# Optimization experiments

Measured on AMD Instinct MI355X. Metric: run time of the kernel, lower is better.

## Reference

```python
import jax, jax.numpy as jnp
import numpy as np

SAME_RANGE = 0.2  # depth tolerance for averaging splats at the same target pixel


def setup_inputs() -> dict:
    key = jax.random.key(0)
    k1, k2, k3 = jax.random.split(key, 3)
    B, C, H, W = 8, 3, 512, 1024
    obj = jax.random.normal(k1, (B, C, H, W), dtype=jnp.float32)
    flow = jax.random.normal(k2, (B, 2, H, W), dtype=jnp.float32)
    depth = jax.random.uniform(k3, (B, 1, H, W), dtype=jnp.float32)
    return {"obj": obj, "flow": flow, "depth": depth}


def reference(obj, flow, depth):
    # Forward-warping splat with per-target-pixel depth (z-buffer) test.
    # For each source pixel: warp by flow, round to nearest target pixel,
    # keep/average contributions whose depth is within same_range of the
    # minimum depth landing on that target pixel.
    B, C, H, W = obj.shape
    # p0: meshgrid with indexing='xy' stacked as (x, y) channels
    gx = jnp.arange(W, dtype=jnp.float32)[None, :]  # [1, W]
    gy = jnp.arange(H, dtype=jnp.float32)[:, None]  # [H, 1]
    p1x = gx + flow[:, 0]  # [B, H, W]
    p1y = gy + flow[:, 1]
    safe_x = jnp.clip(p1x, 0.0, W - 1)
    safe_y = jnp.clip(p1y, 0.0, H - 1)
    xi = jnp.round(safe_x).astype(jnp.int32)
    yi = jnp.round(safe_y).astype(jnp.int32)
    # flat target index, batch-offset so one segment op covers all batches
    boff = (jnp.arange(B, dtype=jnp.int32) * (H * W))[:, None, None]
    idx = (boff + yi * W + xi).reshape(-1)          # [B*H*W]
    d = depth.reshape(-1)                           # [B*H*W] (depth has 1 channel)
    n_seg = B * H * W
    # z-buffer: per-target minimum depth among all splatted source pixels
    dlut = jax.ops.segment_min(d, idx, num_segments=n_seg)
    # contributions within same_range of the winner are averaged
    keep = (d <= dlut[idx] + SAME_RANGE).astype(obj.dtype)  # [B*H*W]
    vals = obj.transpose(0, 2, 3, 1).reshape(-1, C)         # [B*H*W, C]
    sums = jax.ops.segment_sum(vals * keep[:, None], idx, num_segments=n_seg)
    cnts = jax.ops.segment_sum(keep, idx, num_segments=n_seg)
    out = jnp.where(cnts[:, None] > 0, sums / jnp.maximum(cnts[:, None], 1.0), 0.0)
    return out.reshape(B, H, W, C).transpose(0, 3, 1, 2)
```

## Files before the change

### kernel.cpp

```cpp
#include <hip/hip_runtime.h>

#define BB 8
#define CC 3
#define HH 512
#define WW 1024
#define HW (HH * WW)
#define SAME_RANGE 0.2f

#define R 4
#define TX 64
#define TY 32
#define TT (TX * TY)
#define RX (TX + 2 * R)
#define RY (TY + 2 * R)
#define QX (RX / 4)
#define NSLOT (RY * QX)
#define NTHREADS 768
#define CAP 16384
#define D_SENTINEL 0x7F7F7F7F

#define FP_BIAS  16.0f
#define FP_SCALE 524288.0f
#define FP2_BIAS 8.0f
#define FP2_SCALE 8192.0f

__device__ __forceinline__ unsigned int fp_enc(float v) {
    return (unsigned int)__float2uint_rn((v + FP_BIAS) * FP_SCALE);
}
__device__ __forceinline__ unsigned int fp2_enc(float v) {
    return (unsigned int)__float2uint_rn((v + FP2_BIAS) * FP2_SCALE);
}

__device__ __forceinline__ float f4_get(const float4& v, int j) {
    return j == 0 ? v.x : (j == 1 ? v.y : (j == 2 ? v.z : v.w));
}

__global__ __launch_bounds__(NTHREADS) void gather_kernel(
        const float* __restrict__ obj,
        const float* __restrict__ flow,
        const float* __restrict__ depth,
        int* __restrict__ counter,
        float* __restrict__ list,
        float* __restrict__ out) {
    __shared__ int s_dmin[TT];
    __shared__ unsigned int s_a0[TT];
    __shared__ unsigned int s_a1[TT];
    __shared__ unsigned int s_a2c[TT];

    int lin = blockIdx.x + 16 * blockIdx.y + 256 * blockIdx.z;
    int wgid = (lin & 7) * 256 + (lin >> 3);
    int b   = wgid >> 8;
    int rr  = wgid & 255;
    int tx0 = (rr & 15) * TX;
    int ty0 = (rr >> 4) * TY;
    int tid = threadIdx.x;

    for (int i = tid; i < TT; i += NTHREADS) {
        s_dmin[i] = D_SENTINEL;
        s_a0[i] = 0u;
        s_a1[i] = 0u;
        s_a2c[i] = 0u;
    }
    __syncthreads();

    int    c_rem = -1;
    int    c_tl[4] = {-1, -1, -1, -1};
    float  c_d[4] = {0.f, 0.f, 0.f, 0.f};
    float4 c_o0 = make_float4(0.f, 0.f, 0.f, 0.f);
    float4 c_o1 = make_float4(0.f, 0.f, 0.f, 0.f);
    float4 c_o2 = make_float4(0.f, 0.f, 0.f, 0.f);

    if (tid < NSLOT) {
        int sy = tid / QX;
        int sx4 = tid - sy * QX;
        int gy = ty0 - R + sy;
        int gxb = tx0 - R + (sx4 << 2);
        if (gy >= 0 && gy < HH && gxb >= 0 && gxb < WW) {
            int rem = gy * WW + gxb;
            const float4 fx4 = *reinterpret_cast<const float4*>(flow + (size_t)(b * 2 + 0) * HW + rem);
            const float4 fy4 = *reinterpret_cast<const float4*>(flow + (size_t)(b * 2 + 1) * HW + rem);
            const float4 dd4 = *reinterpret_cast<const float4*>(depth + (size_t)b * HW + rem);
            c_o0 = *reinterpret_cast<const float4*>(obj + (size_t)(b * CC + 0) * HW + rem);
            c_o1 = *reinterpret_cast<const float4*>(obj + (size_t)(b * CC + 1) * HW + rem);
            c_o2 = *reinterpret_cast<const float4*>(obj + (size_t)(b * CC + 2) * HW + rem);
            float gyf = (float)gy;
            c_rem = rem;
            #pragma unroll
            for (int j = 0; j < 4; ++j) {
                int px = gxb + j;
                float fx = f4_get(fx4, j) + (float)px;
                float fy = f4_get(fy4, j) + gyf;
                fx = fminf(fmaxf(fx, 0.0f), (float)(WW - 1));
                fy = fminf(fmaxf(fy, 0.0f), (float)(HH - 1));
                int xi = (int)rintf(fx);
                int yi = (int)rintf(fy);
                int ddx = xi - px; if (ddx < 0) ddx = -ddx;
                int ddy = yi - gy; if (ddy < 0) ddy = -ddy;
                float dj = f4_get(dd4, j);
                if (ddx <= R && ddy <= R) {
                    int lx = xi - tx0;
                    int ly = yi - ty0;
                    if (lx >= 0 && lx < TX && ly >= 0 && ly < TY) {
                        int tloc = ly * TX + lx;
                        c_tl[j] = tloc;
                        c_d[j] = dj;
                        atomicMin(&s_dmin[tloc], __float_as_int(dj));
                    }
                } else if (px >= tx0 && px < tx0 + TX &&
                           gy >= ty0 && gy < ty0 + TY) {
                    int pos = atomicAdd(counter, 1);
                    if (pos < CAP) {
                        float* e = list + (size_t)pos * 8;
                        e[0] = __int_as_float(b * HW + yi * WW + xi);
                        e[1] = dj;
                        e[2] = f4_get(c_o0, j);
                        e[3] = f4_get(c_o1, j);
                        e[4] = f4_get(c_o2, j);
                    }
                }
            }
        }
    }
    __syncthreads();

    if (c_rem >= 0) {
        #pragma unroll
        for (int j = 0; j < 4; ++j) {
            int t = c_tl[j];
            if (t >= 0) {
                float thresh = __int_as_float(s_dmin[t]) + SAME_RANGE;
                if (c_d[j] <= thresh) {
                    atomicAdd(&s_a0[t], fp_enc(f4_get(c_o0, j)));
                    atomicAdd(&s_a1[t], fp_enc(f4_get(c_o1, j)));
                    atomicAdd(&s_a2c[t], fp2_enc(f4_get(c_o2, j)) | (1u << 24));
                }
            }
        }
    }
    __syncthreads();

    if (tid < (TT >> 2)) {
        int base = tid << 2;
        int lx = base & (TX - 1);
        int ly = base >> 6;
        int orow = (ty0 + ly) * WW + tx0 + lx;
        float4 r0, r1, r2;
        #pragma unroll
        for (int k = 0; k < 4; ++k) {
            unsigned int a0 = s_a0[base + k];
            unsigned int a1 = s_a1[base + k];
            unsigned int a2c = s_a2c[base + k];
            unsigned int cnt = a2c >> 24;
            float f0 = 0.0f, f1 = 0.0f, f2 = 0.0f;
            if (cnt > 0) {
                float invc = 1.0f / (float)cnt;
                float inv19 = (1.0f / FP_SCALE) * invc;
                f0 = (float)a0 * inv19 - FP_BIAS;
                f1 = (float)a1 * inv19 - FP_BIAS;
                f2 = (float)(a2c & 0x00ffffffu) * ((1.0f / FP2_SCALE) * invc) - FP2_BIAS;
            }
            ((float*)&r0)[k] = f0;
            ((float*)&r1)[k] = f1;
            ((float*)&r2)[k] = f2;
        }
        *reinterpret_cast<float4*>(out + (size_t)(b * CC + 0) * HW + orow) = r0;
        *reinterpret_cast<float4*>(out + (size_t)(b * CC + 1) * HW + orow) = r1;
        *reinterpret_cast<float4*>(out + (size_t)(b * CC + 2) * HW + orow) = r2;
    }
}

__global__ __launch_bounds__(64) void fixup_kernel(
        const float* __restrict__ obj,
        const float* __restrict__ flow,
        const float* __restrict__ depth,
        const int* __restrict__ counter,
        const float* __restrict__ list,
        float* __restrict__ out) {
    int noutl = *counter;
    if (noutl > CAP) noutl = CAP;
    int lane = threadIdx.x;
    for (int o = blockIdx.x; o < noutl; o += gridDim.x) {
        int tidx = __float_as_int(list[(size_t)o * 8]);
        int tb   = tidx >> 19;
        int trem = tidx & (HW - 1);
        int tyy  = trem >> 10;
        int txx  = trem & (WW - 1);
        float cd[2] = {0.0f, 0.0f};
        int   cr[2] = {-1, -1};
        float dmin = 1e30f;
        #pragma unroll
        for (int c = 0; c < 2; ++c) {
            int k = lane + c * 64;
            if (k < 81) {
                int ky = k / 9;
                int sy = tyy - R + ky;
                int sx = txx - R + (k - ky * 9);
                if (sx >= 0 && sx < WW && sy >= 0 && sy < HH) {
                    int srem = sy * WW + sx;
                    float fx = flow[(tb * 2 + 0) * HW + srem] + (float)sx;
                    float fy = flow[(tb * 2 + 1) * HW + srem] + (float)sy;
                    fx = fminf(fmaxf(fx, 0.0f), (float)(WW - 1));
                    fy = fminf(fmaxf(fy, 0.0f), (float)(HH - 1));
                    if ((int)rintf(fx) == txx && (int)rintf(fy) == tyy) {
                        float d = depth[tb * HW + srem];
                        cd[c] = d; cr[c] = srem;
                        dmin = fminf(dmin, d);
                    }
                }
            }
        }
        for (int k = lane; k < noutl; k += 64) {
            const float* e = list + (size_t)k * 8;
            if (__float_as_int(e[0]) == tidx) dmin = fminf(dmin, e[1]);
        }
        #pragma unroll
        for (int m = 32; m >= 1; m >>= 1)
            dmin = fminf(dmin, __shfl_xor(dmin, m));
        float thr = dmin + SAME_RANGE;
        float s0 = 0.0f, s1 = 0.0f, s2 = 0.0f, cnt = 0.0f;
        #pragma unroll
        for (int c = 0; c < 2; ++c) {
            if (cr[c] >= 0 && cd[c] <= thr) {
                s0 += obj[(tb * CC + 0) * HW + cr[c]];
                s1 += obj[(tb * CC + 1) * HW + cr[c]];
                s2 += obj[(tb * CC + 2) * HW + cr[c]];
                cnt += 1.0f;
            }
        }
        for (int k = lane; k < noutl; k += 64) {
            const float* e = list + (size_t)k * 8;
            if (__float_as_int(e[0]) == tidx && e[1] <= thr) {
                s0 += e[2]; s1 += e[3]; s2 += e[4]; cnt += 1.0f;
            }
        }
        #pragma unroll
        for (int m = 32; m >= 1; m >>= 1) {
            s0  += __shfl_xor(s0, m);
            s1  += __shfl_xor(s1, m);
            s2  += __shfl_xor(s2, m);
            cnt += __shfl_xor(cnt, m);
        }
        if (lane == 0) {
            out[(tb * CC + 0) * HW + trem] = s0 / cnt;
            out[(tb * CC + 1) * HW + trem] = s1 / cnt;
            out[(tb * CC + 2) * HW + trem] = s2 / cnt;
        }
    }
}

extern "C" void kernel_launch(void* const* d_in, const int* in_sizes, int n_in,
                              void* d_out, int out_size, void* d_ws, size_t ws_size,
                              hipStream_t stream) {
    const float* obj   = (const float*)d_in[0];
    const float* flow  = (const float*)d_in[1];
    const float* depth = (const float*)d_in[2];
    float* out = (float*)d_out;

    int*   counter = (int*)d_ws;
    float* list    = (float*)((char*)d_ws + 256);

    hipMemsetAsync(counter, 0, sizeof(int), stream);

    gather_kernel<<<dim3(WW / TX, HH / TY, BB), dim3(NTHREADS), 0, stream>>>(
        obj, flow, depth, counter, list, out);

    fixup_kernel<<<dim3(64), dim3(64), 0, stream>>>(
        obj, flow, depth, counter, list, out);
}
```

Measured before the change: 149.0 us.

## Process two horizontal tiles per workgroup with software-pipelined loads

Each workgroup now handles two adjacent 64x32 tiles using separate shared-memory buffers. The second tile's global loads are issued before the first tile's accumulate and store phases, so memory latency overlaps with shared-memory atomic work. The grid is halved and shared memory per block doubles, which may lower occupancy. Halo pixels shared between the two tiles are still loaded twice.

```diff
diff --git a/kernel.cpp b/kernel.cpp
--- a/kernel.cpp
+++ b/kernel.cpp
@@ -11,6 +11,7 @@
 #define TX 64
 #define TY 32
 #define TT (TX * TY)
+#define NT 2
 #define RX (TX + 2 * R)
 #define RY (TY + 2 * R)
 #define QX (RX / 4)
@@ -30,7 +31,6 @@
 __device__ __forceinline__ unsigned int fp2_enc(float v) {
     return (unsigned int)__float2uint_rn((v + FP2_BIAS) * FP2_SCALE);
 }
-
 __device__ __forceinline__ float f4_get(const float4& v, int j) {
     return j == 0 ? v.x : (j == 1 ? v.y : (j == 2 ? v.z : v.w));
 }
@@ -42,97 +42,107 @@
         int* __restrict__ counter,
         float* __restrict__ list,
         float* __restrict__ out) {
-    __shared__ int s_dmin[TT];
-    __shared__ unsigned int s_a0[TT];
-    __shared__ unsigned int s_a1[TT];
-    __shared__ unsigned int s_a2c[TT];
-
-    int lin = blockIdx.x + 16 * blockIdx.y + 256 * blockIdx.z;
-    int wgid = (lin & 7) * 256 + (lin >> 3);
-    int b   = wgid >> 8;
-    int rr  = wgid & 255;
-    int tx0 = (rr & 15) * TX;
-    int ty0 = (rr >> 4) * TY;
+    __shared__ int s_dmin[NT][TT];
+    __shared__ unsigned int s_a0[NT][TT];
+    __shared__ unsigned int s_a1[NT][TT];
+    __shared__ unsigned int s_a2c[NT][TT];
+
+    int lin = blockIdx.x + 8 * blockIdx.y + 128 * blockIdx.z;
+    int wgid = (lin & 7) * 128 + (lin >> 3);
+    int b   = wgid >> 7;
+    int rr  = wgid & 127;
+    int txA = (rr & 7) * (TX * NT);
+    int ty0 = (rr >> 3) * TY;
+    int txB = txA + TX;
     int tid = threadIdx.x;
 
+    int sy  = tid / QX;
+    int sx4 = tid - sy * QX;
+    int gy  = ty0 - R + sy;
+    bool row_ok = (tid < NSLOT) && (gy >= 0) && (gy < HH);
+    float gyf = (float)gy;
+
+    int gxbA = txA - R + (sx4 << 2);
+    bool vA = row_ok && (gxbA >= 0) && (gxbA < WW);
+    int remA = -1;
+    float4 fxA = make_float4(0,0,0,0), fyA = fxA, ddA = fxA;
+    float4 o0A = fxA, o1A = fxA, o2A = fxA;
+    if (vA) {
+        remA = gy * WW + gxbA;
+        fxA = *reinterpret_cast<const float4*>(flow + (size_t)(b * 2 + 0) * HW + remA);
+        fyA = *reinterpret_cast<const float4*>(flow + (size_t)(b * 2 + 1) * HW + remA);
+        ddA = *reinterpret_cast<const float4*>(depth + (size_t)b * HW + remA);
+        o0A = *reinterpret_cast<const float4*>(obj + (size_t)(b * CC + 0) * HW + remA);
+        o1A = *reinterpret_cast<const float4*>(obj + (size_t)(b * CC + 1) * HW + remA);
+        o2A = *reinterpret_cast<const float4*>(obj + (size_t)(b * CC + 2) * HW + remA);
+    }
+
     for (int i = tid; i < TT; i += NTHREADS) {
-        s_dmin[i] = D_SENTINEL;
-        s_a0[i] = 0u;
-        s_a1[i] = 0u;
-        s_a2c[i] = 0u;
-    }
-    __syncthreads();
-
-    int    c_rem = -1;
-    int    c_tl[4] = {-1, -1, -1, -1};
-    float  c_d[4] = {0.f, 0.f, 0.f, 0.f};
-    float4 c_o0 = make_float4(0.f, 0.f, 0.f, 0.f);
-    float4 c_o1 = make_float4(0.f, 0.f, 0.f, 0.f);
-    float4 c_o2 = make_float4(0.f, 0.f, 0.f, 0.f);
-
-    if (tid < NSLOT) {
-        int sy = tid / QX;
-        int sx4 = tid - sy * QX;
-        int gy = ty0 - R + sy;
-        int gxb = tx0 - R + (sx4 << 2);
-        if (gy >= 0 && gy < HH && gxb >= 0 && gxb < WW) {
-            int rem = gy * WW + gxb;
-            const float4 fx4 = *reinterpret_cast<const float4*>(flow + (size_t)(b * 2 + 0) * HW + rem);
-            const float4 fy4 = *reinterpret_cast<const float4*>(flow + (size_t)(b * 2 + 1) * HW + rem);
-            const float4 dd4 = *reinterpret_cast<const float4*>(depth + (size_t)b * HW + rem);
-            c_o0 = *reinterpret_cast<const float4*>(obj + (size_t)(b * CC + 0) * HW + rem);
-            c_o1 = *reinterpret_cast<const float4*>(obj + (size_t)(b * CC + 1) * HW + rem);
-            c_o2 = *reinterpret_cast<const float4*>(obj + (size_t)(b * CC + 2) * HW + rem);
-            float gyf = (float)gy;
-            c_rem = rem;
-            #pragma unroll
-            for (int j = 0; j < 4; ++j) {
-                int px = gxb + j;
-                float fx = f4_get(fx4, j) + (float)px;
-                float fy = f4_get(fy4, j) + gyf;
-                fx = fminf(fmaxf(fx, 0.0f), (float)(WW - 1));
-                fy = fminf(fmaxf(fy, 0.0f), (float)(HH - 1));
-                int xi = (int)rintf(fx);
-                int yi = (int)rintf(fy);
-                int ddx = xi - px; if (ddx < 0) ddx = -ddx;
-                int ddy = yi - gy; if (ddy < 0) ddy = -ddy;
-                float dj = f4_get(dd4, j);
-                if (ddx <= R && ddy <= R) {
-                    int lx = xi - tx0;
-                    int ly = yi - ty0;
-                    if (lx >= 0 && lx < TX && ly >= 0 && ly < TY) {
-                        int tloc = ly * TX + lx;
-                        c_tl[j] = tloc;
-                        c_d[j] = dj;
-                        atomicMin(&s_dmin[tloc], __float_as_int(dj));
-                    }
-                } else if (px >= tx0 && px < tx0 + TX &&
-                           gy >= ty0 && gy < ty0 + TY) {
-                    int pos = atomicAdd(counter, 1);
-                    if (pos < CAP) {
-                        float* e = list + (size_t)pos * 8;
-                        e[0] = __int_as_float(b * HW + yi * WW + xi);
-                        e[1] = dj;
-                        e[2] = f4_get(c_o0, j);
-                        e[3] = f4_get(c_o1, j);
-                        e[4] = f4_get(c_o2, j);
-                    }
-                }
-            }
-        }
-    }
-    __syncthreads();
-
-    if (c_rem >= 0) {
+        s_dmin[0][i] = D_SENTINEL; s_a0[0][i] = 0u; s_a1[0][i] = 0u; s_a2c[0][i] = 0u;
+        s_dmin[1][i] = D_SENTINEL; s_a0[1][i] = 0u; s_a1[1][i] = 0u; s_a2c[1][i] = 0u;
+    }
+    __syncthreads();
+
+    int   tlA[4] = {-1, -1, -1, -1};
+    float dA[4]  = {0.f, 0.f, 0.f, 0.f};
+    if (vA) {
         #pragma unroll
         for (int j = 0; j < 4; ++j) {
-            int t = c_tl[j];
+            int px = gxbA + j;
+            float fx = f4_get(fxA, j) + (float)px;
+            float fy = f4_get(fyA, j) + gyf;
+            fx = fminf(fmaxf(fx, 0.0f), (float)(WW - 1));
+            fy = fminf(fmaxf(fy, 0.0f), (float)(HH - 1));
+            int xi = (int)rintf(fx);
+            int yi = (int)rintf(fy);
+            int ddx = xi - px; if (ddx < 0) ddx = -ddx;
+            int ddy = yi - gy; if (ddy < 0) ddy = -ddy;
+            float dj = f4_get(ddA, j);
+            if (ddx <= R && ddy <= R) {
+                int lx = xi - txA, ly = yi - ty0;
+                if (lx >= 0 && lx < TX && ly >= 0 && ly < TY) {
+                    int t = ly * TX + lx;
+                    tlA[j] = t; dA[j] = dj;
+                    atomicMin(&s_dmin[0][t], __float_as_int(dj));
+                }
+            } else if (px >= txA && px < txA + TX && gy >= ty0 && gy < ty0 + TY) {
+                int pos = atomicAdd(counter, 1);
+                if (pos < CAP) {
+                    float* e = list + (size_t)pos * 8;
+                    e[0] = __int_as_float(b * HW + yi * WW + xi);
+                    e[1] = dj;
+                    e[2] = f4_get(o0A, j); e[3] = f4_get(o1A, j); e[4] = f4_get(o2A, j);
+                }
+            }
+        }
+    }
+    __syncthreads();
+
+    int gxbB = txB - R + (sx4 << 2);
+    bool vB = row_ok && (gxbB >= 0) && (gxbB < WW);
+    int remB = -1;
+    float4 fxB = make_float4(0,0,0,0), fyB = fxB, ddB = fxB;
+    float4 o0B = fxB, o1B = fxB, o2B = fxB;
+    if (vB) {
+        remB = gy * WW + gxbB;
+        fxB = *reinterpret_cast<const float4*>(flow + (size_t)(b * 2 + 0) * HW + remB);
+        fyB = *reinterpret_cast<const float4*>(flow + (size_t)(b * 2 + 1) * HW + remB);
+        ddB = *reinterpret_cast<const float4*>(depth + (size_t)b * HW + remB);
+        o0B = *reinterpret_cast<const float4*>(obj + (size_t)(b * CC + 0) * HW + remB);
+        o1B = *reinterpret_cast<const float4*>(obj + (size_t)(b * CC + 1) * HW + remB);
+        o2B = *reinterpret_cast<const float4*>(obj + (size_t)(b * CC + 2) * HW + remB);
+    }
+
+    if (remA >= 0) {
+        #pragma unroll
+        for (int j = 0; j < 4; ++j) {
+            int t = tlA[j];
             if (t >= 0) {
-                float thresh = __int_as_float(s_dmin[t]) + SAME_RANGE;
-                if (c_d[j] <= thresh) {
-                    atomicAdd(&s_a0[t], fp_enc(f4_get(c_o0, j)));
-                    atomicAdd(&s_a1[t], fp_enc(f4_get(c_o1, j)));
-                    atomicAdd(&s_a2c[t], fp2_enc(f4_get(c_o2, j)) | (1u << 24));
+                float thresh = __int_as_float(s_dmin[0][t]) + SAME_RANGE;
+                if (dA[j] <= thresh) {
+                    atomicAdd(&s_a0[0][t], fp_enc(f4_get(o0A, j)));
+                    atomicAdd(&s_a1[0][t], fp_enc(f4_get(o1A, j)));
+                    atomicAdd(&s_a2c[0][t], fp2_enc(f4_get(o2A, j)) | (1u << 24));
                 }
             }
         }
@@ -143,15 +153,15 @@
         int base = tid << 2;
         int lx = base & (TX - 1);
         int ly = base >> 6;
-        int orow = (ty0 + ly) * WW + tx0 + lx;
+        int orow = (ty0 + ly) * WW + txA + lx;
         float4 r0, r1, r2;
         #pragma unroll
         for (int k = 0; k < 4; ++k) {
-            unsigned int a0 = s_a0[base + k];
-            unsigned int a1 = s_a1[base + k];
-            unsigned int a2c = s_a2c[base + k];
+            unsigned int a0 = s_a0[0][base + k];
+            unsigned int a1 = s_a1[0][base + k];
+            unsigned int a2c = s_a2c[0][base + k];
             unsigned int cnt = a2c >> 24;
-            float f0 = 0.0f, f1 = 0.0f, f2 = 0.0f;
+            float f0 = 0.f, f1 = 0.f, f2 = 0.f;
             if (cnt > 0) {
                 float invc = 1.0f / (float)cnt;
                 float inv19 = (1.0f / FP_SCALE) * invc;
@@ -159,9 +169,84 @@
                 f1 = (float)a1 * inv19 - FP_BIAS;
                 f2 = (float)(a2c & 0x00ffffffu) * ((1.0f / FP2_SCALE) * invc) - FP2_BIAS;
             }
-            ((float*)&r0)[k] = f0;
-            ((float*)&r1)[k] = f1;
-            ((float*)&r2)[k] = f2;
+            ((float*)&r0)[k] = f0; ((float*)&r1)[k] = f1; ((float*)&r2)[k] = f2;
+        }
+        *reinterpret_cast<float4*>(out + (size_t)(b * CC + 0) * HW + orow) = r0;
+        *reinterpret_cast<float4*>(out + (size_t)(b * CC + 1) * HW + orow) = r1;
+        *reinterpret_cast<float4*>(out + (size_t)(b * CC + 2) * HW + orow) = r2;
+    }
+    int   tlB[4] = {-1, -1, -1, -1};
+    float dB[4]  = {0.f, 0.f, 0.f, 0.f};
+    if (vB) {
+        #pragma unroll
+        for (int j = 0; j < 4; ++j) {
+            int px = gxbB + j;
+            float fx = f4_get(fxB, j) + (float)px;
+            float fy = f4_get(fyB, j) + gyf;
+            fx = fminf(fmaxf(fx, 0.0f), (float)(WW - 1));
+            fy = fminf(fmaxf(fy, 0.0f), (float)(HH - 1));
+            int xi = (int)rintf(fx);
+            int yi = (int)rintf(fy);
+            int ddx = xi - px; if (ddx < 0) ddx = -ddx;
+            int ddy = yi - gy; if (ddy < 0) ddy = -ddy;
+            float dj = f4_get(ddB, j);
+            if (ddx <= R && ddy <= R) {
+                int lx = xi - txB, ly = yi - ty0;
+                if (lx >= 0 && lx < TX && ly >= 0 && ly < TY) {
+                    int t = ly * TX + lx;
+                    tlB[j] = t; dB[j] = dj;
+                    atomicMin(&s_dmin[1][t], __float_as_int(dj));
+                }
+            } else if (px >= txB && px < txB + TX && gy >= ty0 && gy < ty0 + TY) {
+                int pos = atomicAdd(counter, 1);
+                if (pos < CAP) {
+                    float* e = list + (size_t)pos * 8;
+                    e[0] = __int_as_float(b * HW + yi * WW + xi);
+                    e[1] = dj;
+                    e[2] = f4_get(o0B, j); e[3] = f4_get(o1B, j); e[4] = f4_get(o2B, j);
+                }
+            }
+        }
+    }
+    __syncthreads();
+
+    if (remB >= 0) {
+        #pragma unroll
+        for (int j = 0; j < 4; ++j) {
+            int t = tlB[j];
+            if (t >= 0) {
+                float thresh = __int_as_float(s_dmin[1][t]) + SAME_RANGE;
+                if (dB[j] <= thresh) {
+                    atomicAdd(&s_a0[1][t], fp_enc(f4_get(o0B, j)));
+                    atomicAdd(&s_a1[1][t], fp_enc(f4_get(o1B, j)));
+                    atomicAdd(&s_a2c[1][t], fp2_enc(f4_get(o2B, j)) | (1u << 24));
+                }
+            }
+        }
+    }
+    __syncthreads();
+
+    if (tid < (TT >> 2)) {
+        int base = tid << 2;
+        int lx = base & (TX - 1);
+        int ly = base >> 6;
+        int orow = (ty0 + ly) * WW + txB + lx;
+        float4 r0, r1, r2;
+        #pragma unroll
+        for (int k = 0; k < 4; ++k) {
+            unsigned int a0 = s_a0[1][base + k];
+            unsigned int a1 = s_a1[1][base + k];
+            unsigned int a2c = s_a2c[1][base + k];
+            unsigned int cnt = a2c >> 24;
+            float f0 = 0.f, f1 = 0.f, f2 = 0.f;
+            if (cnt > 0) {
+                float invc = 1.0f / (float)cnt;
+                float inv19 = (1.0f / FP_SCALE) * invc;
+                f0 = (float)a0 * inv19 - FP_BIAS;
+                f1 = (float)a1 * inv19 - FP_BIAS;
+                f2 = (float)(a2c & 0x00ffffffu) * ((1.0f / FP2_SCALE) * invc) - FP2_BIAS;
+            }
+            ((float*)&r0)[k] = f0; ((float*)&r1)[k] = f1; ((float*)&r2)[k] = f2;
         }
         *reinterpret_cast<float4*>(out + (size_t)(b * CC + 0) * HW + orow) = r0;
         *reinterpret_cast<float4*>(out + (size_t)(b * CC + 1) * HW + orow) = r1;
@@ -261,7 +346,7 @@
 
     hipMemsetAsync(counter, 0, sizeof(int), stream);
 
-    gather_kernel<<<dim3(WW / TX, HH / TY, BB), dim3(NTHREADS), 0, stream>>>(
+    gather_kernel<<<dim3(WW / (TX * NT), HH / TY, BB), dim3(NTHREADS), 0, stream>>>(
         obj, flow, depth, counter, list, out);
 
     fixup_kernel<<<dim3(64), dim3(64), 0, stream>>>(
```

Measured after the change: 152.7 us. +2.5%, slower.
